# Optimization experiments

Hardware: AMD Instinct MI355X
Metric: run time of the kernel (lower is better)

The kernel has to match this reference:

```python
import jax, jax.numpy as jnp
import numpy as np

N, D, H, O, E = 8192, 512, 2048, 512, 8

def setup_inputs() -> dict:
    key = jax.random.key(0)
    ks = jax.random.split(key, 7)
    s = lambda *sh: 1.0 / np.sqrt(sh[-2] if len(sh) > 1 else 1.0)
    x  = jax.random.normal(ks[0], (N, D), dtype=jnp.float32)
    Wr = jax.random.normal(ks[1], (D, E), dtype=jnp.float32) * (1.0 / np.sqrt(D))
    br = jnp.zeros((E,), dtype=jnp.float32)
    W1 = jax.random.normal(ks[2], (E, D, H), dtype=jnp.float32) * (1.0 / np.sqrt(D))
    b1 = jnp.zeros((E, H), dtype=jnp.float32)
    W2 = jax.random.normal(ks[3], (E, H, O), dtype=jnp.float32) * (1.0 / np.sqrt(H))
    b2 = jnp.zeros((E, O), dtype=jnp.float32)
    return {"x": x, "Wr": Wr, "br": br, "W1": W1, "b1": b1, "W2": W2, "b2": b2}


def reference(x, Wr, br, W1, b1, W2, b2):
    # --- supervised router step: Linear -> softmax -> max ---
    router_logits = x @ Wr + br                      # [N, E]
    router_probs = jax.nn.softmax(router_logits, axis=-1)
    p_max = jnp.max(router_probs, axis=-1)           # [N]
    routes = jnp.argmax(router_probs, axis=-1)       # [N] int
    onehot = jax.nn.one_hot(routes, W1.shape[0], dtype=x.dtype)  # [N, E] dispatch mask

    # --- per-expert MLP (dense reference for the gather/compute/scatter pattern) ---
    h = jax.nn.relu(jnp.einsum('nd,edh->enh', x, W1) + b1[:, None, :])  # [E, N, H]
    all_out = jnp.einsum('enh,eho->eno', h, W2) + b2[:, None, :]        # [E, N, O]

    # --- combine: each token takes its routed expert's output ---
    out = jnp.einsum('ne,eno->no', onehot, all_out)  # [N, O]

    # straight-through scaling: value 1 in fwd, routes gradient into router probs
    scale = p_max / jax.lax.stop_gradient(p_max)
    logits = out * scale[:, None]

    counts = jnp.sum(onehot, axis=0)                 # tokens per expert
    return logits, router_probs, counts
```

## Files before the change

kernel.cpp:

```cpp
#include <hip/hip_runtime.h>
#include <hip/hip_bf16.h>
#include <stdint.h>

#define N_TOK 8192
#define DIM   512
#define HID   2048
#define OUTD  512
#define NEXP  8

typedef short  bf16x8 __attribute__((ext_vector_type(8)));
typedef float  f32x4  __attribute__((ext_vector_type(4)));
typedef unsigned short u16x8 __attribute__((ext_vector_type(8)));

#define WS_CNT    0
#define WS_LIST   4096
#define WS_XBF    266240
#define WS_W1T    8654848
#define WS_W2T    25432064
#define WS_H      42209280

__device__ __forceinline__ unsigned short f2bf(float f) {
    uint32_t u = __builtin_bit_cast(uint32_t, f);
    u = (u + 0x7fffu + ((u >> 16) & 1u)) >> 16;
    return (unsigned short)u;
}

__device__ __forceinline__ void gload16(const void* g, void* l) {
    __builtin_amdgcn_global_load_lds(
        (const __attribute__((address_space(1))) unsigned int*)g,
        (__attribute__((address_space(3))) unsigned int*)l, 16, 0, 0);
}

#define MFMA_BF16 __builtin_amdgcn_mfma_f32_16x16x32_bf16

__global__ __launch_bounds__(256) void k1_kernel(
    const float* __restrict__ x, const float* __restrict__ wr, const float* __restrict__ br,
    const float* __restrict__ w1, const float* __restrict__ w2,
    float* __restrict__ probs, int* __restrict__ cnt, int* __restrict__ list,
    unsigned short* __restrict__ xbf, unsigned short* __restrict__ w1t,
    unsigned short* __restrict__ w2t)
{
    const int bid = blockIdx.x, tid = threadIdx.x;
    if (bid < 256) {
        __shared__ int lcnt[NEXP], lbase[NEXP];
        __shared__ int am_l[32], slot_l[32];
        const int w = tid >> 6, lane = tid & 63;
        if (tid < NEXP) lcnt[tid] = 0;
        __syncthreads();
        for (int i = 0; i < 8; i++) {
            const int n = bid * 32 + w * 8 + i;
            float acc[NEXP] = {};
            #pragma unroll
            for (int db = 0; db < 8; db++) {
                const int d = db * 64 + lane;
                const float xv = x[(size_t)n * DIM + d];
                const f32x4 wv0 = *(const f32x4*)&wr[d * 8];
                const f32x4 wv1 = *(const f32x4*)&wr[d * 8 + 4];
                #pragma unroll
                for (int e = 0; e < 4; e++) { acc[e] += xv * wv0[e]; acc[4 + e] += xv * wv1[e]; }
            }
            #pragma unroll
            for (int m = 1; m < 64; m <<= 1)
                #pragma unroll
                for (int e = 0; e < NEXP; e++) acc[e] += __shfl_xor(acc[e], m, 64);
            #pragma unroll
            for (int e = 0; e < NEXP; e++) acc[e] += br[e];
            float mx = acc[0]; int am = 0;
            #pragma unroll
            for (int e = 1; e < NEXP; e++) if (acc[e] > mx) { mx = acc[e]; am = e; }
            float p[NEXP]; float s = 0.f;
            #pragma unroll
            for (int e = 0; e < NEXP; e++) { p[e] = expf(acc[e] - mx); s += p[e]; }
            const float inv = 1.f / s;
            if (lane == 0) {
                f32x4 p0, p1;
                #pragma unroll
                for (int e = 0; e < 4; e++) { p0[e] = p[e] * inv; p1[e] = p[e + 4] * inv; }
                *(f32x4*)&probs[(size_t)n * NEXP]     = p0;
                *(f32x4*)&probs[(size_t)n * NEXP + 4] = p1;
                const int slot = atomicAdd(&lcnt[am], 1);
                am_l[w * 8 + i] = am; slot_l[w * 8 + i] = slot;
            }
        }
        __syncthreads();
        if (tid < NEXP) lbase[tid] = atomicAdd(&cnt[tid], lcnt[tid]);
        __syncthreads();
        if (tid < 32) {
            const int a = am_l[tid];
            list[a * N_TOK + lbase[a] + slot_l[tid]] = bid * 32 + tid;
        }
        const int row = bid * 32 + (tid >> 3), seg = tid & 7;
        const float* src = x + (size_t)row * DIM + seg * 64;
        unsigned short* dst = xbf + (size_t)row * DIM + seg * 64;
        #pragma unroll
        for (int j = 0; j < 8; j++) {
            f32x4 a = *(const f32x4*)&src[j * 8];
            f32x4 b = *(const f32x4*)&src[j * 8 + 4];
            u16x8 o;
            #pragma unroll
            for (int q2 = 0; q2 < 4; q2++) { o[q2] = f2bf(a[q2]); o[4 + q2] = f2bf(b[q2]); }
            *(u16x8*)&dst[j * 8] = o;
        }
    } else {
        __shared__ float t[64][65];
        const float* pin; unsigned short* pout; int C, R, r0, c0;
        if (bid < 2304) {
            const int loc = bid - 256, e = loc >> 8, l2 = loc & 255;
            pin = w1 + (size_t)e * DIM * HID; pout = w1t + (size_t)e * DIM * HID;
            R = DIM; C = HID; r0 = (l2 >> 5) * 64; c0 = (l2 & 31) * 64;
        } else {
            const int loc = bid - 2304, e = loc >> 8, l2 = loc & 255;
            pin = w2 + (size_t)e * HID * OUTD; pout = w2t + (size_t)e * HID * OUTD;
            R = HID; C = OUTD; r0 = (l2 >> 3) * 64; c0 = (l2 & 7) * 64;
        }
        const int r = tid >> 2, q = tid & 3;
        #pragma unroll
        for (int j = 0; j < 4; j++) {
            f32x4 v = *(const f32x4*)&pin[(size_t)(r0 + r) * C + c0 + q * 16 + j * 4];
            #pragma unroll
            for (int i = 0; i < 4; i++) t[r][q * 16 + j * 4 + i] = v[i];
        }
        __syncthreads();
        unsigned short o[16];
        #pragma unroll
        for (int i = 0; i < 16; i++) o[i] = f2bf(t[q * 16 + i][r]);
        unsigned short* dst = &pout[(size_t)(c0 + r) * R + r0 + q * 16];
        *(u16x8*)dst       = *(const u16x8*)&o[0];
        *(u16x8*)(dst + 8) = *(const u16x8*)&o[8];
    }
}

__device__ __forceinline__ int xcd_swizzle(int bid, int nwg, bool& valid) {
    const int xcd = bid & 7, cidx = bid >> 3;
    const int q = nwg >> 3, r = nwg & 7;
    const int csz = q + (xcd < r ? 1 : 0);
    valid = (cidx < csz);
    return (xcd < r ? xcd * (q + 1) : r * (q + 1) + (xcd - r) * q) + cidx;
}

__device__ __forceinline__ void tile_map128(const int* __restrict__ cnt, int tile,
                                            int& e, int& row0, int& bs, int& m_e, int& ntiles) {
    int c[NEXP]; ntiles = 0;
    #pragma unroll
    for (int i = 0; i < NEXP; i++) { c[i] = cnt[i]; ntiles += (c[i] + 127) >> 7; }
    int t = tile, b = 0, ei = 0;
    #pragma unroll
    for (int i = 0; i < NEXP; i++) {
        const int nt = (c[i] + 127) >> 7;
        if (t >= 0 && t < nt) { ei = i; row0 = t << 7; bs = b; m_e = c[i]; }
        t -= nt; b += c[i];
    }
    e = ei;
}

__global__ __launch_bounds__(256) void gemm1_kernel(
    const unsigned short* __restrict__ xbf, const unsigned short* __restrict__ w1t,
    const float* __restrict__ b1, const int* __restrict__ list,
    const int* __restrict__ cnt, unsigned short* __restrict__ h)
{
    int e = 0, row0 = 0, bs = 0, m_e = 0, ntm = 0;
    tile_map128(cnt, 0, e, row0, bs, m_e, ntm);
    const int nwg = ntm * 32;
    bool valid; const int v = xcd_swizzle(blockIdx.x, nwg, valid);
    if (!valid) return;
    const int tile = v >> 5, ntile = v & 31;
    tile_map128(cnt, tile, e, row0, bs, m_e, ntm);
    const int n0 = ntile * 64;

    __shared__ unsigned short ldsA[128 * 64] __attribute__((aligned(16)));
    __shared__ unsigned short ldsB[64 * 64]  __attribute__((aligned(16)));
    __shared__ int ldsTok[128];
    const int tid = threadIdx.x;
    if (tid < 128) { int r = row0 + tid; if (r >= m_e) r = m_e - 1; ldsTok[tid] = list[e * N_TOK + r]; }
    __syncthreads();

    const int gslot = tid & 7;
    const unsigned short* aSrc[4]; const unsigned short* bSrc[2];
    #pragma unroll
    for (int i = 0; i < 4; i++) {
        const int row = (i * 256 + tid) >> 3;
        const int col = ((gslot ^ (row & 7)) << 3);
        aSrc[i] = xbf + (size_t)ldsTok[row] * DIM + col;
    }
    #pragma unroll
    for (int i = 0; i < 2; i++) {
        const int row = (i * 256 + tid) >> 3;
        const int col = ((gslot ^ (row & 7)) << 3);
        bSrc[i] = w1t + ((size_t)e * HID + n0 + row) * DIM + col;
    }

    f32x4 acc[4][2] = {};
    const int lane = tid & 63, wid = tid >> 6;
    const int wm = (wid >> 1) * 64, wn = (wid & 1) * 32;
    const int lrow = lane & 15, gk = lane >> 4, lm = lrow & 7;

    int rowA[4], rowB[2];
    #pragma unroll
    for (int f = 0; f < 4; f++) rowA[f] = (wm + f * 16 + lrow) * 64;
    #pragma unroll
    for (int f = 0; f < 2; f++) rowB[f] = (wn + f * 16 + lrow) * 64;

    for (int t = 0; t < 8; t++) {
        const int k0 = t * 64;
        __syncthreads();
        #pragma unroll
        for (int i = 0; i < 4; i++)
            gload16(aSrc[i] + k0, ldsA + ((i << 8) + (tid & 192)) * 8);
        #pragma unroll
        for (int i = 0; i < 2; i++)
            gload16(bSrc[i] + k0, ldsB + ((i << 8) + (tid & 192)) * 8);
        __syncthreads();
        #pragma unroll
        for (int kk = 0; kk < 2; kk++) {
            bf16x8 av[4], bv[2];
            #pragma unroll
            for (int f = 0; f < 4; f++)
                av[f] = *(const bf16x8*)&ldsA[rowA[f] + ((((kk << 2) + gk) ^ lm) << 3)];
            #pragma unroll
            for (int f = 0; f < 2; f++)
                bv[f] = *(const bf16x8*)&ldsB[rowB[f] + ((((kk << 2) + gk) ^ lm) << 3)];
            #pragma unroll
            for (int mf = 0; mf < 4; mf++)
                #pragma unroll
                for (int nf = 0; nf < 2; nf++)
                    acc[mf][nf] = MFMA_BF16(av[mf], bv[nf], acc[mf][nf], 0, 0, 0);
        }
    }

    const int hbase = bs + row0;
    float bias[2];
    #pragma unroll
    for (int nf = 0; nf < 2; nf++) bias[nf] = b1[e * HID + n0 + wn + nf * 16 + lrow];
    #pragma unroll
    for (int mf = 0; mf < 4; mf++) {
        #pragma unroll
        for (int j = 0; j < 4; j++) {
            const int m = wm + mf * 16 + gk * 4 + j;
            if (row0 + m < m_e) {
                const size_t ro = (size_t)(hbase + m) * HID + n0 + wn;
                #pragma unroll
                for (int nf = 0; nf < 2; nf++) {
                    float vv = acc[mf][nf][j] + bias[nf];
                    h[ro + nf * 16 + lrow] = f2bf(vv > 0.f ? vv : 0.f);
                }
            }
        }
    }
}

__global__ __launch_bounds__(256) void gemm2_kernel(
    const unsigned short* __restrict__ h, const unsigned short* __restrict__ w2t,
    const float* __restrict__ b2, const int* __restrict__ list,
    const int* __restrict__ cnt, float* __restrict__ out, float* __restrict__ counts)
{
    const int tid = threadIdx.x;
    if (blockIdx.x == 0 && tid < NEXP) counts[tid] = (float)cnt[tid];

    int e = 0, row0 = 0, bs = 0, m_e = 0, ntm = 0;
    tile_map128(cnt, 0, e, row0, bs, m_e, ntm);
    const int nwg = ntm * 8;
    bool valid; const int v = xcd_swizzle(blockIdx.x, nwg, valid);
    if (!valid) return;
    const int tile = v >> 3, ntile = v & 7;
    tile_map128(cnt, tile, e, row0, bs, m_e, ntm);
    const int n0 = ntile * 64;

    __shared__ unsigned short ldsA[128 * 128] __attribute__((aligned(16)));
    __shared__ unsigned short ldsB[64 * 128]  __attribute__((aligned(16)));
    __shared__ int ldsTok[128];
    if (tid < 128) { int r = row0 + tid; if (r >= m_e) r = m_e - 1; ldsTok[tid] = list[e * N_TOK + r]; }
    __syncthreads();

    const unsigned short* aSrc[8]; const unsigned short* bSrc[4];
    #pragma unroll
    for (int i = 0; i < 8; i++) {
        const int g = i * 256 + tid, row = g >> 4, gc = g & 15;
        int slot = row0 + row; if (slot >= m_e) slot = m_e - 1;
        aSrc[i] = h + (size_t)(bs + slot) * HID + ((gc ^ (row & 15)) << 3);
    }
    #pragma unroll
    for (int i = 0; i < 4; i++) {
        const int g = i * 256 + tid, row = g >> 4, gc = g & 15;
        bSrc[i] = w2t + ((size_t)e * OUTD + n0 + row) * HID + ((gc ^ (row & 15)) << 3);
    }

    f32x4 acc[4][2] = {};
    const int lane = tid & 63, wid = tid >> 6;
    const int wm = (wid >> 1) * 64, wn = (wid & 1) * 32;
    const int lrow = lane & 15, gk = lane >> 4;

    int rowA[4], rowB[2];
    #pragma unroll
    for (int f = 0; f < 4; f++) rowA[f] = (wm + f * 16 + lrow) * 128;
    #pragma unroll
    for (int f = 0; f < 2; f++) rowB[f] = (wn + f * 16 + lrow) * 128;

    for (int t = 0; t < 16; t++) {
        const int k0 = t * 128;
        __syncthreads();
        #pragma unroll
        for (int i = 0; i < 8; i++)
            gload16(aSrc[i] + k0, ldsA + (i * 256 + tid) * 8);
        #pragma unroll
        for (int i = 0; i < 4; i++)
            gload16(bSrc[i] + k0, ldsB + (i * 256 + tid) * 8);
        __syncthreads();
        #pragma unroll
        for (int kk = 0; kk < 4; kk++) {
            const int gsel = (((kk << 2) + gk) ^ lrow) << 3;
            bf16x8 av[4], bv[2];
            #pragma unroll
            for (int f = 0; f < 4; f++)
                av[f] = *(const bf16x8*)&ldsA[rowA[f] + gsel];
            #pragma unroll
            for (int f = 0; f < 2; f++)
                bv[f] = *(const bf16x8*)&ldsB[rowB[f] + gsel];
            #pragma unroll
            for (int mf = 0; mf < 4; mf++)
                #pragma unroll
                for (int nf = 0; nf < 2; nf++)
                    acc[mf][nf] = MFMA_BF16(av[mf], bv[nf], acc[mf][nf], 0, 0, 0);
        }
    }

    float bias[2];
    #pragma unroll
    for (int nf = 0; nf < 2; nf++) bias[nf] = b2[e * OUTD + n0 + wn + nf * 16 + lrow];
    #pragma unroll
    for (int mf = 0; mf < 4; mf++) {
        #pragma unroll
        for (int j = 0; j < 4; j++) {
            const int m = wm + mf * 16 + gk * 4 + j;
            if (row0 + m < m_e) {
                const size_t ro = (size_t)ldsTok[m] * OUTD + n0 + wn;
                #pragma unroll
                for (int nf = 0; nf < 2; nf++)
                    out[ro + nf * 16 + lrow] = acc[mf][nf][j] + bias[nf];
            }
        }
    }
}

extern "C" void kernel_launch(void* const* d_in, const int* in_sizes, int n_in,
                              void* d_out, int out_size, void* d_ws, size_t ws_size,
                              hipStream_t stream) {
    (void)in_sizes; (void)n_in; (void)out_size; (void)ws_size;
    const float* x  = (const float*)d_in[0];
    const float* wr = (const float*)d_in[1];
    const float* br = (const float*)d_in[2];
    const float* w1 = (const float*)d_in[3];
    const float* b1 = (const float*)d_in[4];
    const float* w2 = (const float*)d_in[5];
    const float* b2 = (const float*)d_in[6];

    float* out    = (float*)d_out;
    float* probs  = out + (size_t)N_TOK * OUTD;
    float* counts = probs + (size_t)N_TOK * NEXP;

    char* ws = (char*)d_ws;
    int* cnt     = (int*)(ws + WS_CNT);
    int* list    = (int*)(ws + WS_LIST);
    unsigned short* xbf = (unsigned short*)(ws + WS_XBF);
    unsigned short* w1t = (unsigned short*)(ws + WS_W1T);
    unsigned short* w2t = (unsigned short*)(ws + WS_W2T);
    unsigned short* hbf = (unsigned short*)(ws + WS_H);

    hipMemsetAsync(cnt, 0, NEXP * sizeof(int), stream);
    k1_kernel<<<4352, 256, 0, stream>>>(x, wr, br, w1, w2, probs, cnt, list, xbf, w1t, w2t);
    gemm1_kernel<<<2272, 256, 0, stream>>>(xbf, w1t, b1, list, cnt, hbf);
    gemm2_kernel<<<568, 256, 0, stream>>>(hbf, w2t, b2, list, cnt, out, counts);
}
```

Before: 102.2 us.

## Triple-buffer LDS in gemm1 with async loads two stages ahead

Replaces the single-buffered load/sync/compute loop in the first expert GEMM with a three-slot LDS ring. Global-to-LDS loads are issued two k-steps ahead, and only the oldest batch is waited on through explicit vmcnt waits and a single barrier per step. Wave priority is raised around the MFMA section. The aim is to hide global load latency behind matrix math. In exchange, LDS use grows to about 72KB per block, which may lower occupancy, and correctness now depends on hand-counted vmcnt values.

```diff
diff --git a/kernel.cpp b/kernel.cpp
--- a/kernel.cpp
+++ b/kernel.cpp
@@ -167,8 +167,8 @@
     tile_map128(cnt, tile, e, row0, bs, m_e, ntm);
     const int n0 = ntile * 64;
 
-    __shared__ unsigned short ldsA[128 * 64] __attribute__((aligned(16)));
-    __shared__ unsigned short ldsB[64 * 64]  __attribute__((aligned(16)));
+    __shared__ unsigned short ldsA[3][128 * 64] __attribute__((aligned(16)));
+    __shared__ unsigned short ldsB[3][64 * 64]  __attribute__((aligned(16)));
     __shared__ int ldsTok[128];
     const int tid = threadIdx.x;
     if (tid < 128) { int r = row0 + tid; if (r >= m_e) r = m_e - 1; ldsTok[tid] = list[e * N_TOK + r]; }
@@ -200,32 +200,53 @@
     #pragma unroll
     for (int f = 0; f < 2; f++) rowB[f] = (wn + f * 16 + lrow) * 64;
 
+    #define STAGE1(slot, k0)                                              \
+        do {                                                              \
+            _Pragma("unroll")                                             \
+            for (int i_ = 0; i_ < 4; i_++)                                \
+                gload16(aSrc[i_] + (k0), &ldsA[slot][((i_ << 8) + (tid & 192)) * 8]); \
+            _Pragma("unroll")                                             \
+            for (int i_ = 0; i_ < 2; i_++)                                \
+                gload16(bSrc[i_] + (k0), &ldsB[slot][((i_ << 8) + (tid & 192)) * 8]); \
+        } while (0)
+
+    STAGE1(0, 0);
+    STAGE1(1, 64);
+    asm volatile("s_waitcnt vmcnt(6)" ::: "memory");
+    __builtin_amdgcn_sched_barrier(0);
+    __builtin_amdgcn_s_barrier();
+
+    #pragma unroll
     for (int t = 0; t < 8; t++) {
-        const int k0 = t * 64;
-        __syncthreads();
-        #pragma unroll
-        for (int i = 0; i < 4; i++)
-            gload16(aSrc[i] + k0, ldsA + ((i << 8) + (tid & 192)) * 8);
-        #pragma unroll
-        for (int i = 0; i < 2; i++)
-            gload16(bSrc[i] + k0, ldsB + ((i << 8) + (tid & 192)) * 8);
-        __syncthreads();
+        const int sl = t % 3;
+        if (t + 2 < 8) {
+            const int s2 = (t + 2) % 3;
+            STAGE1(s2, (t + 2) * 64);
+        }
+        __builtin_amdgcn_s_setprio(1);
         #pragma unroll
         for (int kk = 0; kk < 2; kk++) {
+            const int gsel = (((kk << 2) + gk) ^ lm) << 3;
             bf16x8 av[4], bv[2];
             #pragma unroll
             for (int f = 0; f < 4; f++)
-                av[f] = *(const bf16x8*)&ldsA[rowA[f] + ((((kk << 2) + gk) ^ lm) << 3)];
+                av[f] = *(const bf16x8*)&ldsA[sl][rowA[f] + gsel];
             #pragma unroll
             for (int f = 0; f < 2; f++)
-                bv[f] = *(const bf16x8*)&ldsB[rowB[f] + ((((kk << 2) + gk) ^ lm) << 3)];
+                bv[f] = *(const bf16x8*)&ldsB[sl][rowB[f] + gsel];
             #pragma unroll
             for (int mf = 0; mf < 4; mf++)
                 #pragma unroll
                 for (int nf = 0; nf < 2; nf++)
                     acc[mf][nf] = MFMA_BF16(av[mf], bv[nf], acc[mf][nf], 0, 0, 0);
         }
-    }
+        __builtin_amdgcn_s_setprio(0);
+        if (t <= 5)      asm volatile("s_waitcnt vmcnt(6)" ::: "memory");
+        else if (t == 6) asm volatile("s_waitcnt vmcnt(0)" ::: "memory");
+        __builtin_amdgcn_sched_barrier(0);
+        if (t < 7) __builtin_amdgcn_s_barrier();
+    }
+    #undef STAGE1
 
     const int hbase = bs + row0;
     float bias[2];
```

Result: slower. 111.5 us (+9.1%).
